# Kernel tuning notes

Hardware: AMD Instinct MI355X
Metric: run time of the kernel (lower is better)

The kernel has to match this reference:

```python
import jax, jax.numpy as jnp
from jax import lax
import numpy as np


def setup_inputs() -> dict:
    key = jax.random.key(0)
    k1, k2, k3, k4, k5 = jax.random.split(key, 5)
    bs, m, v, L, P = 2, 16, 16, 40320, 32
    preds = jax.random.normal(k1, (bs, m, v, L), dtype=jnp.float32)
    target = jax.random.normal(k2, (bs, v, L), dtype=jnp.float32)
    weights = jax.random.uniform(k3, (L,), dtype=jnp.float32)
    scale = jax.random.uniform(k4, (v,), dtype=jnp.float32)
    # binary-ish patch masks over grid points (float, as in the torch buffer)
    masks = (jax.random.uniform(k5, (P, L)) < 0.25).astype(jnp.float32)
    return {"preds": preds, "target": target, "weights": weights,
            "scale": scale, "masks": masks, "beta": 1}


def _energy_score(x, y, m, beta):
    # x: (bs, m, D) ensemble, y: (bs, D) observation
    diff = x - y[:, None, :]
    a = jnp.sqrt(jnp.sum(diff * diff, axis=-1))            # (bs, m)
    score_a = jnp.mean(jnp.sum(a ** beta, axis=-1)) / m
    # pairwise distances via Gram trick (cdist p=2)
    sq = jnp.sum(x * x, axis=-1)                            # (bs, m)
    g = jnp.einsum('bid,bjd->bij', x, x)                    # (bs, m, m)
    d2 = jnp.maximum(sq[:, :, None] + sq[:, None, :] - 2.0 * g, 0.0)
    pos = d2 > 0
    d = jnp.where(pos, jnp.sqrt(jnp.where(pos, d2, 1.0)), 0.0)
    score_b = jnp.mean(jnp.sum(d ** beta, axis=(1, 2))) / (2 * m * (m - 1))
    return score_a - score_b


def reference(preds, target, weights, scale, masks, beta):
    beta = float(beta)
    bs, m, v, L = preds.shape
    # buffer scaling as in forward()
    p = preds * scale[None, None, :, None] * weights        # (bs, m, v, L)
    t = target * scale[None, :, None] * weights             # (bs, v, L)

    def body(acc, mask):
        # rearrange 'bs m v latlon -> bs m (latlon v)'
        x = (p * mask).transpose(0, 1, 3, 2).reshape(bs, m, L * v)
        y = (t * mask).transpose(0, 2, 1).reshape(bs, L * v)
        return acc + _energy_score(x, y, m, beta), None

    total, _ = lax.scan(body, jnp.float32(0.0), masks)
    return total
```

## Files before the change

kernel.cpp:

```cpp
#include <hip/hip_runtime.h>
#include <math.h>

#define BS 2
#define M 16
#define V 16
#define NROWB 136
#define NROWS 272
#define PMASK 32
#define KZ 32
#define KSTEPS 1260
#define NWORK 128

typedef __attribute__((ext_vector_type(8))) short bf16x8;
typedef __attribute__((ext_vector_type(4))) float f32x4;

static __device__ __forceinline__ unsigned short f2bf(float x) {
    unsigned int u = __float_as_uint(x);
    unsigned int r = (u + 0x7FFFu + ((u >> 16) & 1u)) >> 16;
    return (unsigned short)r;
}


static __device__ __forceinline__ void k1_stage(
    const float* __restrict__ preds, float* __restrict__ dst,
    int b, int v0, int l0, int L, int lane, int wave)
{
#pragma unroll
    for (int n = 0; n < 4; ++n) {
        int r0 = wave * 16 + n * 4;
        int r = r0 + (lane >> 4);
        int grow = b * 256 + (r >> 2) * 16 + v0 + (r & 3);
        const float* g = preds + (size_t)grow * L + l0 + (lane & 15) * 4;
        __builtin_amdgcn_global_load_lds(
            (const __attribute__((address_space(1))) unsigned int*)g,
            (__attribute__((address_space(3))) unsigned int*)(dst + r0 * 64),
            16, 0, 0);
    }
}

template<int W>
static __device__ __forceinline__ void k1_chunk(
    const float* __restrict__ xsb,
    const float* __restrict__ ty,
    const float* __restrict__ sw,
    int v0, int lane, float* __restrict__ acc)
{
    const int base = (W == 0) ? 0 : 34 * W - 16;
    const int npair = (W == 0) ? 18 : 34;
    const int aoff = (W == 0) ? 16 : 0;

#pragma unroll
    for (int vc = 0; vc < 4; ++vc) {
        const int v = v0 + vc;
        float s = sw[v];
        float x[M];
#pragma unroll
        for (int i = 0; i < M; ++i)
            x[i] = xsb[(i * 4 + vc) * 64 + lane] * s;
        if (W == 0) {
            float y = ty[v];
#pragma unroll
            for (int i = 0; i < M; ++i) {
                float d = x[i] - y;
                acc[i] = fmaf(d, d, acc[i]);
            }
        }
        int k = 0;
#pragma unroll
        for (int i = 0; i < M; ++i) {
#pragma unroll
            for (int j = i + 1; j < M; ++j) {
                if (k >= base && k < base + npair) {
                    float d = x[i] - x[j];
                    acc[aoff + k - base] = fmaf(d, d, acc[aoff + k - base]);
                }
                ++k;
            }
        }
    }
}

__global__ __launch_bounds__(256, 2)
void k1_pairsums(const float* __restrict__ preds, const float* __restrict__ target,
                 const float* __restrict__ weights, const float* __restrict__ scale,
                 const float* __restrict__ masks,
                 unsigned short* __restrict__ S, unsigned short* __restrict__ maskbf,
                 int L)
{
    __shared__ float xs[2][4096];
    int t = (int)threadIdx.x;
    int lane = t & 63, wave = t >> 6;
    int l0 = (int)blockIdx.x * 64;
    int b = (int)blockIdx.y;

    k1_stage(preds, &xs[0][0], b, 0, l0, L, lane, wave);

    float wl = weights[l0 + lane];
    float sw[V];
#pragma unroll
    for (int v = 0; v < V; ++v) sw[v] = scale[v] * wl;
    float ty[V];
    if (wave == 0) {
#pragma unroll
        for (int v = 0; v < V; ++v)
            ty[v] = target[(size_t)(b * V + v) * L + l0 + lane] * sw[v];
    }
    if (b == 0) {
#pragma unroll
        for (int pp = 0; pp < 8; ++pp) {
            int p = wave * 8 + pp;
            maskbf[(size_t)p * L + l0 + lane] =
                (masks[(size_t)p * L + l0 + lane] != 0.0f) ? (unsigned short)0x3F80
                                                           : (unsigned short)0;
        }
    }

    float acc[34];
#pragma unroll
    for (int r = 0; r < 34; ++r) acc[r] = 0.0f;

#pragma unroll
    for (int c = 0; c < 4; ++c) {
        __syncthreads();
        if (c < 3)
            k1_stage(preds, &xs[(c + 1) & 1][0], b, (c + 1) * 4, l0, L, lane, wave);
        const float* xsb = &xs[c & 1][0];
        switch (wave) {
            case 0: k1_chunk<0>(xsb, ty, sw, c * 4, lane, acc); break;
            case 1: k1_chunk<1>(xsb, ty, sw, c * 4, lane, acc); break;
            case 2: k1_chunk<2>(xsb, ty, sw, c * 4, lane, acc); break;
            default: k1_chunk<3>(xsb, ty, sw, c * 4, lane, acc); break;
        }
    }

#pragma unroll
    for (int r = 0; r < 34; ++r)
        S[(size_t)(b * NROWB + 34 * wave + r) * L + l0 + lane] = f2bf(acc[r]);
}

__global__ __launch_bounds__(256, 4)
void k2_mfma(const unsigned short* __restrict__ S,
             const unsigned short* __restrict__ maskbf,
             float* __restrict__ D2p, float* __restrict__ out, int L)
{
    if (blockIdx.x == 0 && blockIdx.y == 0 && threadIdx.x == 0)
        out[0] = 0.0f;

    int lane = (int)(threadIdx.x & 63);
    int wave = (int)(threadIdx.x >> 6);
    int mtile = blockIdx.x;
    int z = blockIdx.y;
    int zw = z * 4 + wave;

    const int q = KSTEPS / NWORK;
    const int rem = KSTEPS % NWORK;
    int start = zw * q + (zw < rem ? zw : rem);
    int cnt = q + (zw < rem ? 1 : 0);

    const unsigned short* Arow =
        S + (size_t)(mtile * 16 + (lane & 15)) * L + (lane >> 4) * 8;
    const unsigned short* B0 =
        maskbf + (size_t)(lane & 15) * L + (lane >> 4) * 8;
    const unsigned short* B1 =
        maskbf + (size_t)(16 + (lane & 15)) * L + (lane >> 4) * 8;

    f32x4 acc0 = {0.f, 0.f, 0.f, 0.f};
    f32x4 acc1 = {0.f, 0.f, 0.f, 0.f};

    for (int s = 0; s < cnt; ++s) {
        int k0 = (start + s) * 32;
        bf16x8 a  = *(const bf16x8*)(Arow + k0);
        bf16x8 b0 = *(const bf16x8*)(B0 + k0);
        bf16x8 b1 = *(const bf16x8*)(B1 + k0);
        acc0 = __builtin_amdgcn_mfma_f32_16x16x32_bf16(a, b0, acc0, 0, 0, 0);
        acc1 = __builtin_amdgcn_mfma_f32_16x16x32_bf16(a, b1, acc1, 0, 0, 0);
    }

    __shared__ float red[4][512];
    int c16 = lane & 15;
#pragma unroll
    for (int reg = 0; reg < 4; ++reg) {
        int r16 = (lane >> 4) * 4 + reg;
        red[wave][r16 * 16 + c16]       = acc0[reg];
        red[wave][256 + r16 * 16 + c16] = acc1[reg];
    }
    __syncthreads();
    int t = (int)threadIdx.x;
#pragma unroll
    for (int u = t; u < 512; u += 256) {
        float v = red[0][u] + red[1][u] + red[2][u] + red[3][u];
        D2p[((size_t)z * 17 + mtile) * 512 + u] = v;
    }
}

__global__ __launch_bounds__(256, 2)
void k3_finalize(const float* __restrict__ D2p, const int* __restrict__ beta_p,
                 float* __restrict__ out)
{
    int t = (int)threadIdx.x;
    int e = blockIdx.x * 256 + t;
    int mtile = e >> 9;
    int flat = e & 511;

    float vbuf[KZ];
#pragma unroll
    for (int z = 0; z < KZ; ++z)
        vbuf[z] = D2p[((size_t)z * 17 + mtile) * 512 + flat];

    float a0 = 0.f, a1 = 0.f, a2 = 0.f, a3 = 0.f;
#pragma unroll
    for (int z = 0; z < KZ; z += 4) {
        a0 += vbuf[z + 0]; a1 += vbuf[z + 1];
        a2 += vbuf[z + 2]; a3 += vbuf[z + 3];
    }
    float d2 = fmaxf((a0 + a1) + (a2 + a3), 0.0f);
    float beta = (float)beta_p[0];
    float d = (beta == 1.0f) ? sqrtf(d2) : powf(d2, 0.5f * beta);

    const float wa = 1.0f / (float)(BS * M);
    const float wb = -1.0f / (float)(BS * M * (M - 1));
    int row = mtile * 16 + ((flat >> 4) & 15);
    int local = row % NROWB;
    float sum = ((local < M) ? wa : wb) * d;

    int lane = t & 63, wv = t >> 6;
#pragma unroll
    for (int off = 32; off > 0; off >>= 1)
        sum += __shfl_down(sum, off, 64);
    __shared__ float red[4];
    if (lane == 0) red[wv] = sum;
    __syncthreads();
    if (t == 0)
        atomicAdd(out, red[0] + red[1] + red[2] + red[3]);
}

extern "C" void kernel_launch(void* const* d_in, const int* in_sizes, int n_in,
                              void* d_out, int out_size, void* d_ws, size_t ws_size,
                              hipStream_t stream)
{
    const float* preds   = (const float*)d_in[0];
    const float* target  = (const float*)d_in[1];
    const float* weights = (const float*)d_in[2];
    const float* scale   = (const float*)d_in[3];
    const float* masks   = (const float*)d_in[4];
    const int*   beta    = (const int*)d_in[5];
    float* out = (float*)d_out;

    int L = in_sizes[2];

    unsigned short* S = (unsigned short*)d_ws;
    size_t s_bytes = (size_t)NROWS * (size_t)L * sizeof(unsigned short);
    unsigned short* maskbf = (unsigned short*)((char*)d_ws + ((s_bytes + 255) & ~(size_t)255));
    size_t m_bytes = (size_t)PMASK * (size_t)L * sizeof(unsigned short);
    float* D2p = (float*)((char*)maskbf + ((m_bytes + 255) & ~(size_t)255));

    dim3 g1(L / 64, BS);
    k1_pairsums<<<g1, 256, 0, stream>>>(preds, target, weights, scale, masks,
                                        S, maskbf, L);

    dim3 g2(17, KZ);
    k2_mfma<<<g2, 256, 0, stream>>>(S, maskbf, D2p, out, L);

    k3_finalize<<<(NROWS * PMASK) / 256, 256, 0, stream>>>(D2p, beta, out);
}
```

Measured before the change: 153.9 us.

## Fuse pair-sum and mask MFMA into one kernel with per-block partials

After: 178.1 us. 15.7% more time.

```diff
diff --git a/kernel.cpp b/kernel.cpp
--- a/kernel.cpp
+++ b/kernel.cpp
@@ -7,19 +7,20 @@
 #define NROWB 136
 #define NROWS 272
 #define PMASK 32
-#define KZ 32
-#define KSTEPS 1260
-#define NWORK 128
+#define NPB 315
+#define CH 2
+#define NE 8704
+#define PBSTRIDE 8704
 
 typedef __attribute__((ext_vector_type(8))) short bf16x8;
 typedef __attribute__((ext_vector_type(4))) float f32x4;
+typedef __attribute__((ext_vector_type(4))) unsigned int u32x4;
 
 static __device__ __forceinline__ unsigned short f2bf(float x) {
     unsigned int u = __float_as_uint(x);
     unsigned int r = (u + 0x7FFFu + ((u >> 16) & 1u)) >> 16;
     return (unsigned short)r;
 }
-
 
 static __device__ __forceinline__ void k1_stage(
     const float* __restrict__ preds, float* __restrict__ dst,
@@ -41,8 +42,9 @@
 template<int W>
 static __device__ __forceinline__ void k1_chunk(
     const float* __restrict__ xsb,
-    const float* __restrict__ ty,
-    const float* __restrict__ sw,
+    const float* __restrict__ targ,
+    const float* __restrict__ scl,
+    float wl,
     int v0, int lane, float* __restrict__ acc)
 {
     const int base = (W == 0) ? 0 : 34 * W - 16;
@@ -52,13 +54,13 @@
 #pragma unroll
     for (int vc = 0; vc < 4; ++vc) {
         const int v = v0 + vc;
-        float s = sw[v];
+        float s = scl[v] * wl;
         float x[M];
 #pragma unroll
         for (int i = 0; i < M; ++i)
             x[i] = xsb[(i * 4 + vc) * 64 + lane] * s;
         if (W == 0) {
-            float y = ty[v];
+            float y = targ[v] * s;
 #pragma unroll
             for (int i = 0; i < M; ++i) {
                 float d = x[i] - y;
@@ -81,149 +83,160 @@
 }
 
 __global__ __launch_bounds__(256, 2)
-void k1_pairsums(const float* __restrict__ preds, const float* __restrict__ target,
-                 const float* __restrict__ weights, const float* __restrict__ scale,
-                 const float* __restrict__ masks,
-                 unsigned short* __restrict__ S, unsigned short* __restrict__ maskbf,
-                 int L)
+void k1_fused(const float* __restrict__ preds, const float* __restrict__ target,
+              const float* __restrict__ weights, const float* __restrict__ scale,
+              const float* __restrict__ masks, float* __restrict__ partial,
+              float* __restrict__ out, int L)
 {
     __shared__ float xs[2][4096];
-    int t = (int)threadIdx.x;
-    int lane = t & 63, wave = t >> 6;
-    int l0 = (int)blockIdx.x * 64;
-    int b = (int)blockIdx.y;
-
-    k1_stage(preds, &xs[0][0], b, 0, l0, L, lane, wave);
-
-    float wl = weights[l0 + lane];
-    float sw[V];
-#pragma unroll
-    for (int v = 0; v < V; ++v) sw[v] = scale[v] * wl;
-    float ty[V];
+    __shared__ unsigned short sld[144 * 64];
+
+    const int t = (int)threadIdx.x;
+    const int lane = t & 63, wave = t >> 6;
+    const int pb = (int)blockIdx.x;
+    const int b  = (int)blockIdx.y;
+
+    if (pb == 0 && b == 0 && t == 0) out[0] = 0.0f;
+
+    ((unsigned int*)sld)[136 * 32 + t] = 0;
+
+    k1_stage(preds, &xs[0][0], b, 0, pb * 64, L, lane, wave);
+
+    float scl[V];
+#pragma unroll
+    for (int v = 0; v < V; ++v) scl[v] = scale[v];
+    float wl = weights[pb * 64 + lane];
+    float targ[V];
     if (wave == 0) {
 #pragma unroll
         for (int v = 0; v < V; ++v)
-            ty[v] = target[(size_t)(b * V + v) * L + l0 + lane] * sw[v];
-    }
-    if (b == 0) {
-#pragma unroll
-        for (int pp = 0; pp < 8; ++pp) {
-            int p = wave * 8 + pp;
-            maskbf[(size_t)p * L + l0 + lane] =
-                (masks[(size_t)p * L + l0 + lane] != 0.0f) ? (unsigned short)0x3F80
-                                                           : (unsigned short)0;
-        }
-    }
+            targ[v] = target[(size_t)(b * V + v) * L + pb * 64 + lane];
+    }
+
+    const int ntile = (wave == 3) ? 3 : 2;
+    f32x4 pacc[3][2];
+#pragma unroll
+    for (int ti = 0; ti < 3; ++ti)
+#pragma unroll
+        for (int pt = 0; pt < 2; ++pt)
+            pacc[ti][pt] = (f32x4){0.f, 0.f, 0.f, 0.f};
 
     float acc[34];
 #pragma unroll
     for (int r = 0; r < 34; ++r) acc[r] = 0.0f;
 
 #pragma unroll
-    for (int c = 0; c < 4; ++c) {
+    for (int c = 0; c < CH; ++c) {
+        const int l0 = (pb + NPB * c) * 64;
+#pragma unroll
+        for (int vq = 0; vq < 4; ++vq) {
+            const int s = c * 4 + vq;
+            __syncthreads();
+            if (s + 1 < 4 * CH) {
+                const int ns = s + 1;
+                k1_stage(preds, &xs[ns & 1][0], b, (ns & 3) * 4,
+                         (pb + NPB * (ns >> 2)) * 64, L, lane, wave);
+            }
+            if (c > 0 && vq == 0) {
+                wl = weights[l0 + lane];
+                if (wave == 0) {
+#pragma unroll
+                    for (int v = 0; v < V; ++v)
+                        targ[v] = target[(size_t)(b * V + v) * L + l0 + lane];
+                }
+#pragma unroll
+                for (int r = 0; r < 34; ++r) acc[r] = 0.0f;
+            }
+            const float* xsb = &xs[s & 1][0];
+            switch (wave) {
+                case 0: k1_chunk<0>(xsb, targ, scl, wl, vq * 4, lane, acc); break;
+                case 1: k1_chunk<1>(xsb, targ, scl, wl, vq * 4, lane, acc); break;
+                case 2: k1_chunk<2>(xsb, targ, scl, wl, vq * 4, lane, acc); break;
+                default: k1_chunk<3>(xsb, targ, scl, wl, vq * 4, lane, acc); break;
+            }
+        }
+
+#pragma unroll
+        for (int r = 0; r < 34; ++r) {
+            const int R = 34 * wave + r;
+            sld[R * 64 + (lane ^ ((R & 7) << 3))] = f2bf(acc[r]);
+        }
         __syncthreads();
-        if (c < 3)
-            k1_stage(preds, &xs[(c + 1) & 1][0], b, (c + 1) * 4, l0, L, lane, wave);
-        const float* xsb = &xs[c & 1][0];
-        switch (wave) {
-            case 0: k1_chunk<0>(xsb, ty, sw, c * 4, lane, acc); break;
-            case 1: k1_chunk<1>(xsb, ty, sw, c * 4, lane, acc); break;
-            case 2: k1_chunk<2>(xsb, ty, sw, c * 4, lane, acc); break;
-            default: k1_chunk<3>(xsb, ty, sw, c * 4, lane, acc); break;
-        }
-    }
-
-#pragma unroll
-    for (int r = 0; r < 34; ++r)
-        S[(size_t)(b * NROWB + 34 * wave + r) * L + l0 + lane] = f2bf(acc[r]);
-}
-
-__global__ __launch_bounds__(256, 4)
-void k2_mfma(const unsigned short* __restrict__ S,
-             const unsigned short* __restrict__ maskbf,
-             float* __restrict__ D2p, float* __restrict__ out, int L)
-{
-    if (blockIdx.x == 0 && blockIdx.y == 0 && threadIdx.x == 0)
-        out[0] = 0.0f;
-
-    int lane = (int)(threadIdx.x & 63);
-    int wave = (int)(threadIdx.x >> 6);
-    int mtile = blockIdx.x;
-    int z = blockIdx.y;
-    int zw = z * 4 + wave;
-
-    const int q = KSTEPS / NWORK;
-    const int rem = KSTEPS % NWORK;
-    int start = zw * q + (zw < rem ? zw : rem);
-    int cnt = q + (zw < rem ? 1 : 0);
-
-    const unsigned short* Arow =
-        S + (size_t)(mtile * 16 + (lane & 15)) * L + (lane >> 4) * 8;
-    const unsigned short* B0 =
-        maskbf + (size_t)(lane & 15) * L + (lane >> 4) * 8;
-    const unsigned short* B1 =
-        maskbf + (size_t)(16 + (lane & 15)) * L + (lane >> 4) * 8;
-
-    f32x4 acc0 = {0.f, 0.f, 0.f, 0.f};
-    f32x4 acc1 = {0.f, 0.f, 0.f, 0.f};
-
-    for (int s = 0; s < cnt; ++s) {
-        int k0 = (start + s) * 32;
-        bf16x8 a  = *(const bf16x8*)(Arow + k0);
-        bf16x8 b0 = *(const bf16x8*)(B0 + k0);
-        bf16x8 b1 = *(const bf16x8*)(B1 + k0);
-        acc0 = __builtin_amdgcn_mfma_f32_16x16x32_bf16(a, b0, acc0, 0, 0, 0);
-        acc1 = __builtin_amdgcn_mfma_f32_16x16x32_bf16(a, b1, acc1, 0, 0, 0);
-    }
-
-    __shared__ float red[4][512];
-    int c16 = lane & 15;
-#pragma unroll
-    for (int reg = 0; reg < 4; ++reg) {
-        int r16 = (lane >> 4) * 4 + reg;
-        red[wave][r16 * 16 + c16]       = acc0[reg];
-        red[wave][256 + r16 * 16 + c16] = acc1[reg];
-    }
-    __syncthreads();
-    int t = (int)threadIdx.x;
-#pragma unroll
-    for (int u = t; u < 512; u += 256) {
-        float v = red[0][u] + red[1][u] + red[2][u] + red[3][u];
-        D2p[((size_t)z * 17 + mtile) * 512 + u] = v;
+
+#pragma unroll
+        for (int ks = 0; ks < 2; ++ks) {
+            bf16x8 bfr[2];
+#pragma unroll
+            for (int pt = 0; pt < 2; ++pt) {
+                const float* mp = masks + (size_t)(pt * 16 + (lane & 15)) * L
+                                + l0 + ks * 32 + (lane >> 4) * 8;
+                u32x4 m0 = *(const u32x4*)mp;
+                u32x4 m1 = *(const u32x4*)(mp + 4);
+                union { unsigned int u[4]; bf16x8 v; } bb;
+                bb.u[0] = __builtin_amdgcn_perm(m0.y, m0.x, 0x07060302);
+                bb.u[1] = __builtin_amdgcn_perm(m0.w, m0.z, 0x07060302);
+                bb.u[2] = __builtin_amdgcn_perm(m1.y, m1.x, 0x07060302);
+                bb.u[3] = __builtin_amdgcn_perm(m1.w, m1.z, 0x07060302);
+                bfr[pt] = bb.v;
+            }
+#pragma unroll
+            for (int ti = 0; ti < 3; ++ti) {
+                if (ti >= ntile) continue;
+                const int tile = (ti == 2) ? 8 : (wave + ti * 4);
+                const bf16x8 a = *(const bf16x8*)&sld[
+                    (tile * 16 + (lane & 15)) * 64 +
+                    ((ks * 32 + (lane >> 4) * 8) ^ ((lane & 7) << 3))];
+                pacc[ti][0] = __builtin_amdgcn_mfma_f32_16x16x32_bf16(
+                    a, bfr[0], pacc[ti][0], 0, 0, 0);
+                pacc[ti][1] = __builtin_amdgcn_mfma_f32_16x16x32_bf16(
+                    a, bfr[1], pacc[ti][1], 0, 0, 0);
+            }
+        }
+    }
+
+    float* P = partial + (size_t)(pb * 2 + b) * (NROWB * PMASK);
+#pragma unroll
+    for (int ti = 0; ti < 3; ++ti) {
+        if (ti >= ntile) continue;
+        const int tile = (ti == 2) ? 8 : (wave + ti * 4);
+#pragma unroll
+        for (int pt = 0; pt < 2; ++pt)
+#pragma unroll
+            for (int reg = 0; reg < 4; ++reg) {
+                const int row = tile * 16 + (lane >> 4) * 4 + reg;
+                if (row < NROWB)
+                    P[row * 32 + pt * 16 + (lane & 15)] = pacc[ti][pt][reg];
+            }
     }
 }
 
 __global__ __launch_bounds__(256, 2)
-void k3_finalize(const float* __restrict__ D2p, const int* __restrict__ beta_p,
+void k3_finalize(const float* __restrict__ P, const int* __restrict__ beta_p,
                  float* __restrict__ out)
 {
-    int t = (int)threadIdx.x;
-    int e = blockIdx.x * 256 + t;
-    int mtile = e >> 9;
-    int flat = e & 511;
-
-    float vbuf[KZ];
-#pragma unroll
-    for (int z = 0; z < KZ; ++z)
-        vbuf[z] = D2p[((size_t)z * 17 + mtile) * 512 + flat];
-
-    float a0 = 0.f, a1 = 0.f, a2 = 0.f, a3 = 0.f;
-#pragma unroll
-    for (int z = 0; z < KZ; z += 4) {
-        a0 += vbuf[z + 0]; a1 += vbuf[z + 1];
-        a2 += vbuf[z + 2]; a3 += vbuf[z + 3];
-    }
-    float d2 = fmaxf((a0 + a1) + (a2 + a3), 0.0f);
+    const int t = (int)threadIdx.x;
+    const int e = (int)blockIdx.x * 256 + t;
+
+    float a0 = 0.f, a1 = 0.f, a2 = 0.f, a3 = 0.f, a4 = 0.f;
+    const float* p = P + e;
+    for (int q = 0; q < NPB; q += 5) {
+        a0 += p[(size_t)(q    ) * PBSTRIDE];
+        a1 += p[(size_t)(q + 1) * PBSTRIDE];
+        a2 += p[(size_t)(q + 2) * PBSTRIDE];
+        a3 += p[(size_t)(q + 3) * PBSTRIDE];
+        a4 += p[(size_t)(q + 4) * PBSTRIDE];
+    }
+    float d2 = fmaxf(((a0 + a1) + (a2 + a3)) + a4, 0.0f);
     float beta = (float)beta_p[0];
     float d = (beta == 1.0f) ? sqrtf(d2) : powf(d2, 0.5f * beta);
 
     const float wa = 1.0f / (float)(BS * M);
     const float wb = -1.0f / (float)(BS * M * (M - 1));
-    int row = mtile * 16 + ((flat >> 4) & 15);
-    int local = row % NROWB;
+    const int row_g = e >> 5;
+    const int local = row_g % NROWB;
     float sum = ((local < M) ? wa : wb) * d;
 
-    int lane = t & 63, wv = t >> 6;
+    const int lane = t & 63, wv = t >> 6;
 #pragma unroll
     for (int off = 32; off > 0; off >>= 1)
         sum += __shfl_down(sum, off, 64);
@@ -248,18 +261,11 @@
 
     int L = in_sizes[2];
 
-    unsigned short* S = (unsigned short*)d_ws;
-    size_t s_bytes = (size_t)NROWS * (size_t)L * sizeof(unsigned short);
-    unsigned short* maskbf = (unsigned short*)((char*)d_ws + ((s_bytes + 255) & ~(size_t)255));
-    size_t m_bytes = (size_t)PMASK * (size_t)L * sizeof(unsigned short);
-    float* D2p = (float*)((char*)maskbf + ((m_bytes + 255) & ~(size_t)255));
-
-    dim3 g1(L / 64, BS);
-    k1_pairsums<<<g1, 256, 0, stream>>>(preds, target, weights, scale, masks,
-                                        S, maskbf, L);
-
-    dim3 g2(17, KZ);
-    k2_mfma<<<g2, 256, 0, stream>>>(S, maskbf, D2p, out, L);
-
-    k3_finalize<<<(NROWS * PMASK) / 256, 256, 0, stream>>>(D2p, beta, out);
-}
+    float* partial = (float*)d_ws;
+
+    dim3 g1(NPB, BS);
+    k1_fused<<<g1, 256, 0, stream>>>(preds, target, weights, scale, masks,
+                                     partial, out, L);
+
+    k3_finalize<<<NE / 256, 256, 0, stream>>>(partial, beta, out);
+}
```
